# Optimization experiments

Hardware: AMD Instinct MI355X
Metric: run time of the kernel (lower is better)

Reference implementation:

```python
import jax, jax.numpy as jnp
import numpy as np

N_E = 4096
E_DIM = 512
BETA = 0.25


def setup_inputs() -> dict:
    key = jax.random.key(0)
    k1, k2 = jax.random.split(key)
    z = jax.random.normal(k1, (32, 512, E_DIM), dtype=jnp.float32)
    # embedding.weight ~ U(-1/n_e, 1/n_e)
    emb = jax.random.uniform(k2, (N_E, E_DIM), dtype=jnp.float32,
                             minval=-1.0 / N_E, maxval=1.0 / N_E)
    return {"z": z, "emb": emb}


def reference(z, emb):
    B, S, D = z.shape
    zf = z.reshape(-1, D)  # (N, D)
    # squared L2 distances: ||z||^2 + ||e||^2 - 2 z @ e^T  -> (N, n_e)
    d = (jnp.sum(zf * zf, axis=1, keepdims=True)
         + jnp.sum(emb * emb, axis=1)
         - 2.0 * jnp.matmul(zf, emb.T))
    idx = jnp.argmin(d, axis=1)  # (N,)
    z_q = emb[idx].reshape(z.shape)

    # commitment / codebook loss (detach = stop_gradient)
    loss = (jnp.mean((z_q - jax.lax.stop_gradient(z)) ** 2)
            + BETA * jnp.mean((jax.lax.stop_gradient(z_q) - z) ** 2))

    # straight-through estimator
    z_q_st = z + jax.lax.stop_gradient(z_q - z)

    # perplexity via codeword usage histogram (equiv. to mean of one-hots)
    N = zf.shape[0]
    counts = jnp.zeros((N_E,), dtype=z.dtype).at[idx].add(1.0)
    e_mean = counts / N
    perplexity = jnp.exp(-jnp.sum(e_mean * jnp.log(e_mean + 1e-10)))

    return (loss, z_q_st, idx, perplexity)
```

## Files before the change

### kernel.cpp

```cpp
#include <hip/hip_runtime.h>
#include <math.h>

#define NROWS 16384
#define DDIM  512
#define NE    4096
#define NZ    (NROWS * DDIM)
#define MAXC  64
#define MARGIN 2e-3f

typedef __attribute__((ext_vector_type(8))) short bf16x8;
typedef __attribute__((ext_vector_type(4))) float f32x4;

__device__ __forceinline__ float sqr_rn(float x) { return __fmul_rn(x, x); }
__device__ __forceinline__ ushort f2bf(float f) {
    const unsigned u = __float_as_uint(f);
    return (ushort)((u + 0x7fffu + ((u >> 16) & 1u)) >> 16);
}
__device__ __forceinline__ unsigned pack2(float a, float b) {
    return (unsigned)f2bf(a) | ((unsigned)f2bf(b) << 16);
}
__device__ __forceinline__ void glds16(const void* g, void* l) {
    __builtin_amdgcn_global_load_lds(
        (const __attribute__((address_space(1))) unsigned int*)g,
        (__attribute__((address_space(3))) unsigned int*)l, 16, 0, 0);
}

__global__ void k_prep(const float* __restrict__ z, const float* __restrict__ emb,
                       ushort* __restrict__ zh, ushort* __restrict__ eh,
                       float* __restrict__ znorm, float* __restrict__ bnorm,
                       unsigned* __restrict__ counts) {
    if (blockIdx.x < 1024) {
        const int lane = threadIdx.x & 63;
        const int c = (int)((blockIdx.x * 256 + threadIdx.x) >> 6);
        const float4* p = (const float4*)(emb + (size_t)c * DDIM);
        const float4 v0 = p[lane * 2], v1 = p[lane * 2 + 1];
        uint4 w; w.x = pack2(v0.x, v0.y); w.y = pack2(v0.z, v0.w);
        w.z = pack2(v1.x, v1.y); w.w = pack2(v1.z, v1.w);
        *(uint4*)(eh + (size_t)c * DDIM + lane * 8) = w;
        float s = v0.x*v0.x + v0.y*v0.y + v0.z*v0.z + v0.w*v0.w
                + v1.x*v1.x + v1.y*v1.y + v1.z*v1.z + v1.w*v1.w;
        #pragma unroll
        for (int m = 32; m; m >>= 1) s += __shfl_xor(s, m);
        if (lane == 0) { bnorm[c] = s; counts[c] = 0u; }
    } else {
        const int t = (int)((blockIdx.x - 1024) * 256 + threadIdx.x);
        const int row = t >> 2, blk = t & 3;
        const float4* p = (const float4*)(z + (size_t)row * DDIM + blk * 128);
        ushort* zo = zh + (size_t)row * DDIM + blk * 128;
        float4 v0 = p[0], v1 = p[1];
        {
            uint4 w; w.x = pack2(v0.x, v0.y); w.y = pack2(v0.z, v0.w);
            w.z = pack2(v1.x, v1.y); w.w = pack2(v1.z, v1.w);
            *(uint4*)zo = w;
        }
        float r[8];
        r[0] = sqr_rn(v0.x); r[1] = sqr_rn(v0.y); r[2] = sqr_rn(v0.z); r[3] = sqr_rn(v0.w);
        r[4] = sqr_rn(v1.x); r[5] = sqr_rn(v1.y); r[6] = sqr_rn(v1.z); r[7] = sqr_rn(v1.w);
        #pragma unroll
        for (int i = 1; i < 16; ++i) {
            v0 = p[2 * i]; v1 = p[2 * i + 1];
            uint4 w; w.x = pack2(v0.x, v0.y); w.y = pack2(v0.z, v0.w);
            w.z = pack2(v1.x, v1.y); w.w = pack2(v1.z, v1.w);
            *(uint4*)(zo + i * 8) = w;
            r[0] = __fadd_rn(r[0], sqr_rn(v0.x)); r[1] = __fadd_rn(r[1], sqr_rn(v0.y));
            r[2] = __fadd_rn(r[2], sqr_rn(v0.z)); r[3] = __fadd_rn(r[3], sqr_rn(v0.w));
            r[4] = __fadd_rn(r[4], sqr_rn(v1.x)); r[5] = __fadd_rn(r[5], sqr_rn(v1.y));
            r[6] = __fadd_rn(r[6], sqr_rn(v1.z)); r[7] = __fadd_rn(r[7], sqr_rn(v1.w));
        }
        const float B = __fadd_rn(__fadd_rn(__fadd_rn(r[0], r[1]), __fadd_rn(r[2], r[3])),
                                  __fadd_rn(__fadd_rn(r[4], r[5]), __fadd_rn(r[6], r[7])));
        const float s01 = __fadd_rn(B, __shfl_xor(B, 1));
        const float zn  = __fadd_rn(s01, __shfl_xor(s01, 2));
        if (blk == 0) znorm[row] = zn;
    }
}

template <int USE_BLK>
__global__ __launch_bounds__(256) void k_mfma(const ushort* __restrict__ zh,
                                              const ushort* __restrict__ eh,
                                              const float* __restrict__ bnorm,
                                              ushort* __restrict__ sbuf,
                                              float* __restrict__ rowblkmin) {
    __shared__ ushort Af[8 * 512];
    __shared__ ushort Bf[8 * 512];
    const int tid = threadIdx.x;
    const int lane = tid & 63;
    const int w = tid >> 6;
    const int wrow = (w >> 1) * 64, wcol = (w & 1) * 64;
    const int rbase = blockIdx.x * 128, cbase = blockIdx.y * 128;
    const int r16 = lane & 15, g4 = (lane >> 4) * 4;
    const int k8 = (lane >> 4) * 8;
    const int c0 = 2 * w, c1 = c0 + 1;

    const ushort* gA0 = zh + (size_t)(rbase + 16 * c0 + r16) * DDIM + k8;
    const ushort* gA1 = zh + (size_t)(rbase + 16 * c1 + r16) * DDIM + k8;
    const ushort* gB0 = eh + (size_t)(cbase + 16 * c0 + r16) * DDIM + k8;
    const ushort* gB1 = eh + (size_t)(cbase + 16 * c1 + r16) * DDIM + k8;
    ushort* lA0 = &Af[c0 * 512]; ushort* lA1 = &Af[c1 * 512];
    ushort* lB0 = &Bf[c0 * 512]; ushort* lB1 = &Bf[c1 * 512];

    f32x4 acc[4][4];
    #pragma unroll
    for (int i = 0; i < 4; ++i)
        #pragma unroll
        for (int j = 0; j < 4; ++j) acc[i][j] = (f32x4){0.f, 0.f, 0.f, 0.f};

    for (int kb = 0; kb < DDIM; kb += 32) {
        __syncthreads();
        glds16(gA0 + kb, lA0);
        glds16(gA1 + kb, lA1);
        glds16(gB0 + kb, lB0);
        glds16(gB1 + kb, lB1);
        __syncthreads();
        bf16x8 af[4], bf[4];
        #pragma unroll
        for (int f = 0; f < 4; ++f) {
            af[f] = *(const bf16x8*)&Af[((wrow >> 4) + f) * 512 + lane * 8];
            bf[f] = *(const bf16x8*)&Bf[((wcol >> 4) + f) * 512 + lane * 8];
        }
        #pragma unroll
        for (int fi = 0; fi < 4; ++fi)
            #pragma unroll
            for (int fj = 0; fj < 4; ++fj)
                acc[fi][fj] = __builtin_amdgcn_mfma_f32_16x16x32_bf16(
                    af[fi], bf[fj], acc[fi][fj], 0, 0, 0);
    }

    float bn[4];
    #pragma unroll
    for (int fj = 0; fj < 4; ++fj) bn[fj] = bnorm[cbase + wcol + fj * 16 + r16];

    #pragma unroll
    for (int fi = 0; fi < 4; ++fi) {
        #pragma unroll
        for (int r = 0; r < 4; ++r) {
            const int row = rbase + wrow + fi * 16 + g4 + r;
            float s[4];
            #pragma unroll
            for (int fj = 0; fj < 4; ++fj) s[fj] = fmaf(-2.f, acc[fi][fj][r], bn[fj]);
            uint2* sp = (uint2*)(sbuf + (size_t)row * NE + cbase + wcol);
            sp[r16] = make_uint2(pack2(s[0], s[1]), pack2(s[2], s[3]));
            if (USE_BLK) {
                float m = fminf(fminf(s[0], s[1]), fminf(s[2], s[3]));
                #pragma unroll
                for (int x = 1; x < 16; x <<= 1) m = fminf(m, __shfl_xor(m, x));
                if (r16 == 0)
                    rowblkmin[(size_t)row * 64 + blockIdx.y * 2 + (w & 1)] = m;
            }
        }
    }
}

__device__ __forceinline__ unsigned long long exact_key(const float4* __restrict__ zp4,
                                                        const float* __restrict__ emb,
                                                        const float* __restrict__ bnorm,
                                                        float zn, int c) {
    const float4* ep4 = (const float4*)(emb + (size_t)c * DDIM);
    float acc = 0.f;
    #pragma unroll 8
    for (int q = 0; q < DDIM / 4; ++q) {
        const float4 zv = zp4[q];
        const float4 ev = ep4[q];
        acc = fmaf(zv.x, ev.x, acc);
        acc = fmaf(zv.y, ev.y, acc);
        acc = fmaf(zv.z, ev.z, acc);
        acc = fmaf(zv.w, ev.w, acc);
    }
    const float s = __fsub_rn(__fadd_rn(zn, bnorm[c]), __fmul_rn(2.f, acc));
    return ((unsigned long long)__float_as_uint(s) << 32) | (unsigned)c;
}

template <int GUIDED>
__global__ void k_pg(const ushort* __restrict__ sbuf, const float* __restrict__ rowblkmin,
                     const float* __restrict__ z, const float* __restrict__ emb,
                     const float* __restrict__ znorm, const float* __restrict__ bnorm,
                     float* __restrict__ out, unsigned* __restrict__ counts,
                     float* __restrict__ d2buf) {
    __shared__ int candL[4][MAXC];
    __shared__ unsigned cntL[4];
    const int lane = threadIdx.x & 63;
    const int w = threadIdx.x >> 6;
    const int row = blockIdx.x * 4 + w;
    if (threadIdx.x < 4) cntL[threadIdx.x] = 0u;
    __syncthreads();

    if (GUIDED) {
        const float bm = rowblkmin[(size_t)row * 64 + lane];
        float gmin = bm;
        #pragma unroll
        for (int m = 32; m; m >>= 1) gmin = fminf(gmin, __shfl_xor(gmin, m));
        const float thr = gmin + MARGIN;
        unsigned long long bmask = __ballot(bm <= thr);
        while (bmask) {
            const int b = __builtin_ctzll(bmask); bmask &= bmask - 1;
            const float val = __uint_as_float(
                (unsigned)sbuf[(size_t)row * NE + b * 64 + lane] << 16);
            if (val <= thr) {
                const unsigned slot = atomicAdd(&cntL[w], 1u);
                if (slot < MAXC)
                    candL[w][slot] = b * 64 + (lane & 3) * 16 + (lane >> 2);
            }
        }
    } else {
        const uint4* p = (const uint4*)(sbuf + (size_t)row * NE);
        uint4 v[8];
        #pragma unroll
        for (int j = 0; j < 8; ++j) v[j] = p[j * 64 + lane];
        float mn = INFINITY;
        #pragma unroll
        for (int j = 0; j < 8; ++j) {
            const unsigned* u = (const unsigned*)&v[j];
            #pragma unroll
            for (int q = 0; q < 4; ++q) {
                mn = fminf(mn, __uint_as_float(u[q] << 16));
                mn = fminf(mn, __uint_as_float(u[q] & 0xffff0000u));
            }
        }
        #pragma unroll
        for (int m = 32; m; m >>= 1) mn = fminf(mn, __shfl_xor(mn, m));
        const float thr = mn + MARGIN;
        #pragma unroll
        for (int j = 0; j < 8; ++j) {
            const unsigned* u = (const unsigned*)&v[j];
            #pragma unroll
            for (int q = 0; q < 4; ++q) {
                #pragma unroll
                for (int hi = 0; hi < 2; ++hi) {
                    const float val = __uint_as_float(hi ? (u[q] & 0xffff0000u)
                                                        : (u[q] << 16));
                    if (val <= thr) {
                        const int pos = j * 512 + lane * 8 + q * 2 + hi;
                        const int inb = pos & 63;
                        const unsigned slot = atomicAdd(&cntL[w], 1u);
                        if (slot < MAXC)
                            candL[w][slot] = (pos >> 6) * 64 + (inb & 3) * 16 + (inb >> 2);
                    }
                }
            }
        }
    }
    __syncthreads();

    const int cnt = (int)cntL[w];
    int id;
    if (cnt == 1) {
        id = candL[w][0] & (NE - 1);
    } else {
        const float zn = znorm[row];
        const float4* zp4 = (const float4*)(z + (size_t)row * DDIM);
        unsigned long long best = ~0ULL;
        if (cnt >= 2 && cnt <= MAXC) {
            if (lane < cnt)
                best = exact_key(zp4, emb, bnorm, zn, candL[w][lane] & (NE - 1));
        } else {
            for (int c = lane; c < NE; c += 64) {
                const unsigned long long k = exact_key(zp4, emb, bnorm, zn, c);
                if (k < best) best = k;
            }
        }
        #pragma unroll
        for (int m = 32; m; m >>= 1) {
            const unsigned long long ov = __shfl_xor(best, m);
            if (ov < best) best = ov;
        }
        id = (int)(__shfl(best, 0) & (unsigned long long)(NE - 1));
    }

    const float* zp = z + (size_t)row * DDIM;
    const float* ep = emb + (size_t)id * DDIM;
    float* op = out + 1 + (size_t)row * DDIM;
    float d2 = 0.f;
    #pragma unroll
    for (int m = 0; m < 8; ++m) {
        const int k = m * 64 + lane;
        const float e = ep[k];
        const float zv = zp[k];
        const float t = e - zv;
        op[k] = zv + t;
        d2 = fmaf(t, t, d2);
    }
    #pragma unroll
    for (int m = 32; m; m >>= 1) d2 += __shfl_xor(d2, m);
    if (lane == 0) {
        atomicAdd(&counts[id], 1u);
        d2buf[row] = d2;
        out[1 + (size_t)NZ + row] = (float)id;
    }
}

__global__ void k_final(const float* __restrict__ d2buf, const unsigned* __restrict__ counts,
                        float* __restrict__ out) {
    __shared__ double sh[256];
    __shared__ float  shf[256];
    const int tid = threadIdx.x;
    double ent = 0.0;
    for (int i = tid; i < NE; i += 256) {
        const double p = (double)counts[i] / (double)NROWS;
        ent += p * log(p + 1e-10);
    }
    float sse = 0.f;
    for (int i = tid; i < NROWS; i += 256) sse += d2buf[i];
    sh[tid] = ent; shf[tid] = sse;
    __syncthreads();
    for (int s = 128; s; s >>= 1) {
        if (tid < s) { sh[tid] += sh[tid + s]; shf[tid] += shf[tid + s]; }
        __syncthreads();
    }
    if (tid == 0) {
        out[0] = 1.25f * (shf[0] / (float)NZ);
        out[1 + (size_t)NZ + NROWS] = (float)exp(-sh[0]);
    }
}

extern "C" void kernel_launch(void* const* d_in, const int* in_sizes, int n_in,
                              void* d_out, int out_size, void* d_ws, size_t ws_size,
                              hipStream_t stream) {
    const float* z   = (const float*)d_in[0];
    const float* emb = (const float*)d_in[1];
    float* out = (float*)d_out;
    char* ws = (char*)d_ws;

    ushort* zh = (ushort*)(out + 4);
    ushort* eh = (ushort*)(out + 4 + 4194304);

    size_t off = 0;
    float*    bnorm  = (float*)(ws + off); off += (size_t)NE * 4;
    unsigned* counts = (unsigned*)(ws + off); off += (size_t)NE * 4;
    float*    d2buf  = (float*)(ws + off); off += (size_t)NROWS * 4;
    float*    znorm  = (float*)(ws + off); off += (size_t)NROWS * 4;
    ushort*   sbuf   = (ushort*)(ws + off); off += (size_t)NROWS * NE * 2;
    float*    rowblkmin = (float*)(ws + off); off += (size_t)NROWS * 64 * 4;
    const bool guided = ws_size >= off;

    k_prep<<<1280, 256, 0, stream>>>(z, emb, zh, eh, znorm, bnorm, counts);
    if (guided) {
        k_mfma<1><<<dim3(NROWS / 128, NE / 128), 256, 0, stream>>>(zh, eh, bnorm, sbuf, rowblkmin);
        k_pg<1><<<NROWS / 4, 256, 0, stream>>>(sbuf, rowblkmin, z, emb, znorm, bnorm, out, counts, d2buf);
    } else {
        k_mfma<0><<<dim3(NROWS / 128, NE / 128), 256, 0, stream>>>(zh, eh, bnorm, sbuf, rowblkmin);
        k_pg<0><<<NROWS / 4, 256, 0, stream>>>(sbuf, rowblkmin, z, emb, znorm, bnorm, out, counts, d2buf);
    }
    k_final<<<1, 256, 0, stream>>>(d2buf, counts, out);
}
```

Before: 292.7 us.

## Replace full bf16 score buffer with per-row candidate lists filtered in GEMM epilogue

The GEMM epilogue no longer writes the full 16384x4096 bf16 distance matrix. It keeps per-subblock minima and appends near-minimum candidates (bf16 score plus index) to a per-row list through a global atomic counter. The argmin kernel reads only these candidates, filters them against the global row minimum and rescores the survivors in exact fp32. The K loop also stages 64 instead of 32 per iteration, halving the barriers. This trades the ~128MB score write and readback for global atomics in the epilogue, larger LDS tiles, a workspace-size fallback that was dropped, and a full 4096-code scan for any row that overflows the candidate cap.

```diff
diff --git a/kernel.cpp b/kernel.cpp
--- a/kernel.cpp
+++ b/kernel.cpp
@@ -5,7 +5,7 @@
 #define DDIM  512
 #define NE    4096
 #define NZ    (NROWS * DDIM)
-#define MAXC  64
+#define CAP   512
 #define MARGIN 2e-3f
 
 typedef __attribute__((ext_vector_type(8))) short bf16x8;
@@ -28,7 +28,7 @@
 __global__ void k_prep(const float* __restrict__ z, const float* __restrict__ emb,
                        ushort* __restrict__ zh, ushort* __restrict__ eh,
                        float* __restrict__ znorm, float* __restrict__ bnorm,
-                       unsigned* __restrict__ counts) {
+                       unsigned* __restrict__ counts, unsigned* __restrict__ ccnt) {
     if (blockIdx.x < 1024) {
         const int lane = threadIdx.x & 63;
         const int c = (int)((blockIdx.x * 256 + threadIdx.x) >> 6);
@@ -72,17 +72,18 @@
         const float s01 = __fadd_rn(B, __shfl_xor(B, 1));
         const float zn  = __fadd_rn(s01, __shfl_xor(s01, 2));
         if (blk == 0) znorm[row] = zn;
-    }
-}
-
-template <int USE_BLK>
+        if (t < NROWS) ccnt[t] = 0u;
+    }
+}
+
 __global__ __launch_bounds__(256) void k_mfma(const ushort* __restrict__ zh,
                                               const ushort* __restrict__ eh,
                                               const float* __restrict__ bnorm,
-                                              ushort* __restrict__ sbuf,
-                                              float* __restrict__ rowblkmin) {
-    __shared__ ushort Af[8 * 512];
-    __shared__ ushort Bf[8 * 512];
+                                              float* __restrict__ rowblkmin,
+                                              unsigned* __restrict__ ccnt,
+                                              unsigned* __restrict__ cand) {
+    __shared__ ushort Af[8 * 1024];
+    __shared__ ushort Bf[8 * 1024];
     const int tid = threadIdx.x;
     const int lane = tid & 63;
     const int w = tid >> 6;
@@ -96,8 +97,6 @@
     const ushort* gA1 = zh + (size_t)(rbase + 16 * c1 + r16) * DDIM + k8;
     const ushort* gB0 = eh + (size_t)(cbase + 16 * c0 + r16) * DDIM + k8;
     const ushort* gB1 = eh + (size_t)(cbase + 16 * c1 + r16) * DDIM + k8;
-    ushort* lA0 = &Af[c0 * 512]; ushort* lA1 = &Af[c1 * 512];
-    ushort* lB0 = &Bf[c0 * 512]; ushort* lB1 = &Bf[c1 * 512];
 
     f32x4 acc[4][4];
     #pragma unroll
@@ -105,25 +104,32 @@
         #pragma unroll
         for (int j = 0; j < 4; ++j) acc[i][j] = (f32x4){0.f, 0.f, 0.f, 0.f};
 
-    for (int kb = 0; kb < DDIM; kb += 32) {
+    for (int kb = 0; kb < DDIM; kb += 64) {
         __syncthreads();
-        glds16(gA0 + kb, lA0);
-        glds16(gA1 + kb, lA1);
-        glds16(gB0 + kb, lB0);
-        glds16(gB1 + kb, lB1);
+        glds16(gA0 + kb,      &Af[c0 * 1024]);
+        glds16(gA0 + kb + 32, &Af[c0 * 1024 + 512]);
+        glds16(gA1 + kb,      &Af[c1 * 1024]);
+        glds16(gA1 + kb + 32, &Af[c1 * 1024 + 512]);
+        glds16(gB0 + kb,      &Bf[c0 * 1024]);
+        glds16(gB0 + kb + 32, &Bf[c0 * 1024 + 512]);
+        glds16(gB1 + kb,      &Bf[c1 * 1024]);
+        glds16(gB1 + kb + 32, &Bf[c1 * 1024 + 512]);
         __syncthreads();
-        bf16x8 af[4], bf[4];
-        #pragma unroll
-        for (int f = 0; f < 4; ++f) {
-            af[f] = *(const bf16x8*)&Af[((wrow >> 4) + f) * 512 + lane * 8];
-            bf[f] = *(const bf16x8*)&Bf[((wcol >> 4) + f) * 512 + lane * 8];
-        }
-        #pragma unroll
-        for (int fi = 0; fi < 4; ++fi)
+        #pragma unroll
+        for (int s = 0; s < 2; ++s) {
+            bf16x8 af[4], bf[4];
             #pragma unroll
-            for (int fj = 0; fj < 4; ++fj)
-                acc[fi][fj] = __builtin_amdgcn_mfma_f32_16x16x32_bf16(
-                    af[fi], bf[fj], acc[fi][fj], 0, 0, 0);
+            for (int f = 0; f < 4; ++f) {
+                af[f] = *(const bf16x8*)&Af[((wrow >> 4) + f) * 1024 + s * 512 + lane * 8];
+                bf[f] = *(const bf16x8*)&Bf[((wcol >> 4) + f) * 1024 + s * 512 + lane * 8];
+            }
+            #pragma unroll
+            for (int fi = 0; fi < 4; ++fi)
+                #pragma unroll
+                for (int fj = 0; fj < 4; ++fj)
+                    acc[fi][fj] = __builtin_amdgcn_mfma_f32_16x16x32_bf16(
+                        af[fi], bf[fj], acc[fi][fj], 0, 0, 0);
+        }
     }
 
     float bn[4];
@@ -138,14 +144,25 @@
             float s[4];
             #pragma unroll
             for (int fj = 0; fj < 4; ++fj) s[fj] = fmaf(-2.f, acc[fi][fj][r], bn[fj]);
-            uint2* sp = (uint2*)(sbuf + (size_t)row * NE + cbase + wcol);
-            sp[r16] = make_uint2(pack2(s[0], s[1]), pack2(s[2], s[3]));
-            if (USE_BLK) {
-                float m = fminf(fminf(s[0], s[1]), fminf(s[2], s[3]));
+            float m = fminf(fminf(s[0], s[1]), fminf(s[2], s[3]));
+            #pragma unroll
+            for (int x = 1; x < 16; x <<= 1) m = fminf(m, __shfl_xor(m, x));
+            if (r16 == 0)
+                rowblkmin[(size_t)row * 64 + blockIdx.y * 2 + (w & 1)] = m;
+            const float thrA = m + MARGIN;
+            int h = (s[0] <= thrA) + (s[1] <= thrA) + (s[2] <= thrA) + (s[3] <= thrA);
+            if (h) {
+                unsigned base = atomicAdd(&ccnt[row], (unsigned)h);
                 #pragma unroll
-                for (int x = 1; x < 16; x <<= 1) m = fminf(m, __shfl_xor(m, x));
-                if (r16 == 0)
-                    rowblkmin[(size_t)row * 64 + blockIdx.y * 2 + (w & 1)] = m;
+                for (int fj = 0; fj < 4; ++fj) {
+                    if (s[fj] <= thrA) {
+                        if (base < CAP)
+                            cand[(size_t)row * CAP + base] =
+                                ((unsigned)f2bf(s[fj]) << 16) |
+                                (unsigned)(cbase + wcol + fj * 16 + r16);
+                        ++base;
+                    }
+                }
             }
         }
     }
@@ -170,88 +187,51 @@
     return ((unsigned long long)__float_as_uint(s) << 32) | (unsigned)c;
 }
 
-template <int GUIDED>
-__global__ void k_pg(const ushort* __restrict__ sbuf, const float* __restrict__ rowblkmin,
-                     const float* __restrict__ z, const float* __restrict__ emb,
-                     const float* __restrict__ znorm, const float* __restrict__ bnorm,
-                     float* __restrict__ out, unsigned* __restrict__ counts,
-                     float* __restrict__ d2buf) {
-    __shared__ int candL[4][MAXC];
-    __shared__ unsigned cntL[4];
+__global__ void k_pg(const float* __restrict__ rowblkmin, const unsigned* __restrict__ ccnt,
+                     const unsigned* __restrict__ cand, const float* __restrict__ z,
+                     const float* __restrict__ emb, const float* __restrict__ znorm,
+                     const float* __restrict__ bnorm, float* __restrict__ out,
+                     unsigned* __restrict__ counts, float* __restrict__ d2buf) {
+    __shared__ int keepL[4][64];
+    __shared__ unsigned kcnt[4];
     const int lane = threadIdx.x & 63;
     const int w = threadIdx.x >> 6;
     const int row = blockIdx.x * 4 + w;
-    if (threadIdx.x < 4) cntL[threadIdx.x] = 0u;
+    if (threadIdx.x < 4) kcnt[threadIdx.x] = 0u;
     __syncthreads();
 
-    if (GUIDED) {
-        const float bm = rowblkmin[(size_t)row * 64 + lane];
-        float gmin = bm;
-        #pragma unroll
-        for (int m = 32; m; m >>= 1) gmin = fminf(gmin, __shfl_xor(gmin, m));
-        const float thr = gmin + MARGIN;
-        unsigned long long bmask = __ballot(bm <= thr);
-        while (bmask) {
-            const int b = __builtin_ctzll(bmask); bmask &= bmask - 1;
-            const float val = __uint_as_float(
-                (unsigned)sbuf[(size_t)row * NE + b * 64 + lane] << 16);
-            if (val <= thr) {
-                const unsigned slot = atomicAdd(&cntL[w], 1u);
-                if (slot < MAXC)
-                    candL[w][slot] = b * 64 + (lane & 3) * 16 + (lane >> 2);
-            }
-        }
-    } else {
-        const uint4* p = (const uint4*)(sbuf + (size_t)row * NE);
-        uint4 v[8];
-        #pragma unroll
-        for (int j = 0; j < 8; ++j) v[j] = p[j * 64 + lane];
-        float mn = INFINITY;
-        #pragma unroll
-        for (int j = 0; j < 8; ++j) {
-            const unsigned* u = (const unsigned*)&v[j];
-            #pragma unroll
-            for (int q = 0; q < 4; ++q) {
-                mn = fminf(mn, __uint_as_float(u[q] << 16));
-                mn = fminf(mn, __uint_as_float(u[q] & 0xffff0000u));
-            }
-        }
-        #pragma unroll
-        for (int m = 32; m; m >>= 1) mn = fminf(mn, __shfl_xor(mn, m));
-        const float thr = mn + MARGIN;
-        #pragma unroll
-        for (int j = 0; j < 8; ++j) {
-            const unsigned* u = (const unsigned*)&v[j];
-            #pragma unroll
-            for (int q = 0; q < 4; ++q) {
-                #pragma unroll
-                for (int hi = 0; hi < 2; ++hi) {
-                    const float val = __uint_as_float(hi ? (u[q] & 0xffff0000u)
-                                                        : (u[q] << 16));
-                    if (val <= thr) {
-                        const int pos = j * 512 + lane * 8 + q * 2 + hi;
-                        const int inb = pos & 63;
-                        const unsigned slot = atomicAdd(&cntL[w], 1u);
-                        if (slot < MAXC)
-                            candL[w][slot] = (pos >> 6) * 64 + (inb & 3) * 16 + (inb >> 2);
-                    }
+    const float bm = rowblkmin[(size_t)row * 64 + lane];
+    float gmin = bm;
+    #pragma unroll
+    for (int m = 32; m; m >>= 1) gmin = fminf(gmin, __shfl_xor(gmin, m));
+    const float thr = gmin + MARGIN;
+
+    const int cnt = (int)ccnt[row];
+    if (cnt <= CAP) {
+        for (int base = 0; base < cnt; base += 64) {
+            const int i = base + lane;
+            if (i < cnt) {
+                const unsigned u = cand[(size_t)row * CAP + i];
+                if (__uint_as_float(u & 0xffff0000u) <= thr) {
+                    const unsigned slot = atomicAdd(&kcnt[w], 1u);
+                    if (slot < 64) keepL[w][slot] = (int)(u & 0xffffu);
                 }
             }
         }
     }
     __syncthreads();
 
-    const int cnt = (int)cntL[w];
+    const int kept = (int)kcnt[w];
     int id;
-    if (cnt == 1) {
-        id = candL[w][0] & (NE - 1);
+    if (cnt <= CAP && kept == 1) {
+        id = keepL[w][0] & (NE - 1);
     } else {
         const float zn = znorm[row];
         const float4* zp4 = (const float4*)(z + (size_t)row * DDIM);
         unsigned long long best = ~0ULL;
-        if (cnt >= 2 && cnt <= MAXC) {
-            if (lane < cnt)
-                best = exact_key(zp4, emb, bnorm, zn, candL[w][lane] & (NE - 1));
+        if (cnt <= CAP && kept >= 1 && kept <= 64) {
+            if (lane < kept)
+                best = exact_key(zp4, emb, bnorm, zn, keepL[w][lane] & (NE - 1));
         } else {
             for (int c = lane; c < NE; c += 64) {
                 const unsigned long long k = exact_key(zp4, emb, bnorm, zn, c);
@@ -328,17 +308,12 @@
     unsigned* counts = (unsigned*)(ws + off); off += (size_t)NE * 4;
     float*    d2buf  = (float*)(ws + off); off += (size_t)NROWS * 4;
     float*    znorm  = (float*)(ws + off); off += (size_t)NROWS * 4;
-    ushort*   sbuf   = (ushort*)(ws + off); off += (size_t)NROWS * NE * 2;
+    unsigned* ccnt   = (unsigned*)(ws + off); off += (size_t)NROWS * 4;
     float*    rowblkmin = (float*)(ws + off); off += (size_t)NROWS * 64 * 4;
-    const bool guided = ws_size >= off;
-
-    k_prep<<<1280, 256, 0, stream>>>(z, emb, zh, eh, znorm, bnorm, counts);
-    if (guided) {
-        k_mfma<1><<<dim3(NROWS / 128, NE / 128), 256, 0, stream>>>(zh, eh, bnorm, sbuf, rowblkmin);
-        k_pg<1><<<NROWS / 4, 256, 0, stream>>>(sbuf, rowblkmin, z, emb, znorm, bnorm, out, counts, d2buf);
-    } else {
-        k_mfma<0><<<dim3(NROWS / 128, NE / 128), 256, 0, stream>>>(zh, eh, bnorm, sbuf, rowblkmin);
-        k_pg<0><<<NROWS / 4, 256, 0, stream>>>(sbuf, rowblkmin, z, emb, znorm, bnorm, out, counts, d2buf);
-    }
+    unsigned* cand   = (unsigned*)(ws + off); off += (size_t)NROWS * CAP * 4;
+
+    k_prep<<<1280, 256, 0, stream>>>(z, emb, zh, eh, znorm, bnorm, counts, ccnt);
+    k_mfma<<<dim3(NROWS / 128, NE / 128), 256, 0, stream>>>(zh, eh, bnorm, rowblkmin, ccnt, cand);
+    k_pg<<<NROWS / 4, 256, 0, stream>>>(rowblkmin, ccnt, cand, z, emb, znorm, bnorm, out, counts, d2buf);
     k_final<<<1, 256, 0, stream>>>(d2buf, counts, out);
 }
```

After: 444.2 us. 51.8% more time.
